# Performance work log

Hardware: AMD Instinct MI355X
Metric: run time of the kernel (lower is better)

Reference implementation:

```python
import jax, jax.numpy as jnp
import numpy as np

N = 100000      # nodes per node type (asset, zone)
E = 1000000     # edges per edge type
HID = 64        # hidden_dim
HEADS = 2
CH = HID // HEADS  # 32, GATConv out_channels per head
L = 2           # num_layers
A = 64          # action_count
NG = 6          # global features
FW = 2 * HID + NG  # 134 feature width for heads


def _gat(xs_in, xd_in, W, a_src, a_dst, bias, src, dst, n_dst):
    """PyG GATConv (v1, add_self_loops=False, concat=True) for one edge type.
    xs_in: [Ns, HID] source feats, xd_in: [Nd, HID] dest feats (same lin weight W).
    Returns [n_dst, HEADS*CH]."""
    xs = (xs_in @ W).reshape(-1, HEADS, CH)
    xd = (xd_in @ W).reshape(-1, HEADS, CH)
    al_s = jnp.einsum('nhc,hc->nh', xs, a_src)
    al_d = jnp.einsum('nhc,hc->nh', xd, a_dst)
    al = jax.nn.leaky_relu(al_s[src] + al_d[dst], 0.2)       # [E, H]
    mx = jax.ops.segment_max(al, dst, num_segments=n_dst)    # segment softmax (stable)
    mx = jnp.where(jnp.isfinite(mx), mx, 0.0)                # empty segments
    ex = jnp.exp(al - mx[dst])
    den = jax.ops.segment_sum(ex, dst, num_segments=n_dst)
    w = ex / (den[dst] + 1e-16)                              # PyG softmax eps
    msg = xs[src] * w[:, :, None]                            # [E, H, C]
    out = jax.ops.segment_sum(msg.reshape(msg.shape[0], HEADS * CH), dst, num_segments=n_dst)
    return out + bias


def setup_inputs() -> dict:
    key = jax.random.key(0)
    ks = jax.random.split(key, 24)
    s = 0.05
    inp = {
        'x_asset': jax.random.normal(ks[0], (N, 16), jnp.float32),
        'x_zone': jax.random.normal(ks[1], (N, 32), jnp.float32),
        'ei_zz': jax.random.randint(ks[2], (2, E), 0, N, dtype=jnp.int32),
        'ei_az': jax.random.randint(ks[3], (2, E), 0, N, dtype=jnp.int32),
        'ei_za': jax.random.randint(ks[4], (2, E), 0, N, dtype=jnp.int32),
        'gvec': jax.random.uniform(ks[5], (NG,), jnp.float32),
        'mask': jax.random.randint(ks[6], (A,), 0, 2) == 1,
        'proj_W_asset': jax.random.normal(ks[7], (16, HID), jnp.float32) * s,
        'proj_b_asset': jnp.zeros((HID,), jnp.float32),
        'proj_W_zone': jax.random.normal(ks[8], (32, HID), jnp.float32) * s,
        'proj_b_zone': jnp.zeros((HID,), jnp.float32),
        'gat_W': jax.random.normal(ks[9], (L, 3, HID, HID), jnp.float32) * s,
        'gat_asrc': jax.random.normal(ks[10], (L, 3, HEADS, CH), jnp.float32) * s,
        'gat_adst': jax.random.normal(ks[11], (L, 3, HEADS, CH), jnp.float32) * s,
        'gat_bias': jnp.zeros((L, 3, HID), jnp.float32),
        'actor_W1': jax.random.normal(ks[12], (FW, HID), jnp.float32) * s,
        'actor_b1': jnp.zeros((HID,), jnp.float32),
        'actor_W2': jax.random.normal(ks[13], (HID, A), jnp.float32) * s,
        'actor_b2': jnp.zeros((A,), jnp.float32),
        'critic_W1': jax.random.normal(ks[14], (FW, HID), jnp.float32) * s,
        'critic_b1': jnp.zeros((HID,), jnp.float32),
        'critic_W2': jax.random.normal(ks[15], (HID, 1), jnp.float32) * s,
        'critic_b2': jnp.zeros((1,), jnp.float32),
    }
    return inp


def reference(x_asset, x_zone, ei_zz, ei_az, ei_za, gvec, mask,
              proj_W_asset, proj_b_asset, proj_W_zone, proj_b_zone,
              gat_W, gat_asrc, gat_adst, gat_bias,
              actor_W1, actor_b1, actor_W2, actor_b2,
              critic_W1, critic_b1, critic_W2, critic_b2):
    # input projections per node type
    ha = x_asset @ proj_W_asset + proj_b_asset   # [N, HID]
    hz = x_zone @ proj_W_zone + proj_b_zone      # [N, HID]
    # HeteroConv stack: edge types 0=(zone,near,zone) 1=(asset,in,zone) 2=(zone,contains,asset), aggr='sum'
    for l in range(L):
        z_zz = _gat(hz, hz, gat_W[l, 0], gat_asrc[l, 0], gat_adst[l, 0], gat_bias[l, 0], ei_zz[0], ei_zz[1], N)
        z_az = _gat(ha, hz, gat_W[l, 1], gat_asrc[l, 1], gat_adst[l, 1], gat_bias[l, 1], ei_az[0], ei_az[1], N)
        a_za = _gat(hz, ha, gat_W[l, 2], gat_asrc[l, 2], gat_adst[l, 2], gat_bias[l, 2], ei_za[0], ei_za[1], N)
        hz = jax.nn.relu(z_zz + z_az)
        ha = jax.nn.relu(a_za)
    # mean pool per node type, sorted order: asset, zone
    pooled = jnp.concatenate([ha.mean(axis=0), hz.mean(axis=0)])
    feats = jnp.concatenate([pooled, gvec])      # [FW]
    logits = jax.nn.relu(feats @ actor_W1 + actor_b1) @ actor_W2 + actor_b2   # [A]
    value = jax.nn.relu(feats @ critic_W1 + critic_b1) @ critic_W2 + critic_b2  # [1]
    m = jnp.where(mask.any(), mask, jnp.ones_like(mask))
    masked = jnp.where(m, logits, -jnp.inf)
    return jnp.concatenate([masked, value])      # [A+1]: masked logits + value
```

## Files before the change

kernel.cpp:

```cpp
#include <hip/hip_runtime.h>
#include <math.h>

#define CE 8192
#define BSH 9
#define BMAXB 512
#define ASTR 104
#define DSTR 72

typedef __attribute__((ext_vector_type(8))) short bf16x8;
typedef __attribute__((ext_vector_type(4))) float f32x4;
typedef __attribute__((ext_vector_type(2))) float f32x2;

__device__ __forceinline__ unsigned short f2bf(float f) {
    unsigned u = __float_as_uint(f);
    u += 0x7fffu + ((u >> 16) & 1u);
    return (unsigned short)(u >> 16);
}
__device__ __forceinline__ float bf2f(unsigned short u) {
    return __uint_as_float(((unsigned)u) << 16);
}

__global__ __launch_bounds__(256) void gemm2_k(const float* __restrict__ Xa,
                                               const float* __restrict__ Xz,
                                               const float* __restrict__ Wa,
                                               const float* __restrict__ Wz,
                                               const float* __restrict__ ba,
                                               const float* __restrict__ bz,
                                               unsigned short* __restrict__ outa,
                                               unsigned short* __restrict__ outz,
                                               int n) {
    const int y = blockIdx.y;
    const float* X = y ? Xz : Xa;
    const float* W = y ? Wz : Wa;
    const float* bias = y ? bz : ba;
    unsigned short* outb = y ? outz : outa;
    const int kshift = y ? 5 : 4;
    const int K = 1 << kshift;

    __shared__ float sXt[64 * 68];
    __shared__ float sW[64 * 64];
    __shared__ float sB[64];
    const int tid = threadIdx.x;
    const int row0 = blockIdx.x * 64;

    for (int i = tid * 4; i < 64 * K; i += 1024) {
        int r = i >> kshift, k = i & (K - 1);
        int row = row0 + r;
        float4 v = make_float4(0.f, 0.f, 0.f, 0.f);
        if (row < n) v = *(const float4*)(X + (size_t)row * K + k);
        sXt[(k + 0) * 68 + r] = v.x;
        sXt[(k + 1) * 68 + r] = v.y;
        sXt[(k + 2) * 68 + r] = v.z;
        sXt[(k + 3) * 68 + r] = v.w;
    }
    for (int i = tid * 4; i < K * 64; i += 1024)
        *(float4*)(sW + i) = *(const float4*)(W + i);
    if (tid < 64) sB[tid] = bias[tid];
    __syncthreads();

    const int tc = tid & 15, tr = tid >> 4;
    float acc[4][4] = {};
#pragma unroll 8
    for (int k = 0; k < K; ++k) {
        float4 a = *(const float4*)(sXt + k * 68 + tr * 4);
        float4 b = *(const float4*)(sW + k * 64 + tc * 4);
        acc[0][0] += a.x * b.x; acc[0][1] += a.x * b.y; acc[0][2] += a.x * b.z; acc[0][3] += a.x * b.w;
        acc[1][0] += a.y * b.x; acc[1][1] += a.y * b.y; acc[1][2] += a.y * b.z; acc[1][3] += a.y * b.w;
        acc[2][0] += a.z * b.x; acc[2][1] += a.z * b.y; acc[2][2] += a.z * b.z; acc[2][3] += a.z * b.w;
        acc[3][0] += a.w * b.x; acc[3][1] += a.w * b.y; acc[3][2] += a.w * b.z; acc[3][3] += a.w * b.w;
    }
#pragma unroll
    for (int i = 0; i < 4; ++i) {
        int row = row0 + tr * 4 + i;
        if (row < n) {
            float4 o;
            o.x = acc[i][0] + sB[tc * 4 + 0];
            o.y = acc[i][1] + sB[tc * 4 + 1];
            o.z = acc[i][2] + sB[tc * 4 + 2];
            o.w = acc[i][3] + sB[tc * 4 + 3];
            ushort4 v4 = make_ushort4(f2bf(o.x), f2bf(o.y), f2bf(o.z), f2bf(o.w));
            *(ushort4*)(outb + (size_t)row * 64 + tc * 4) = v4;
        }
    }
}

__global__ void prep_k(const float* __restrict__ gW, const float* __restrict__ gad,
                       unsigned short* __restrict__ Wbt, float* __restrict__ Wd3All) {
    int b = blockIdx.x;
    int t = threadIdx.x;
    if (b < 6) {
        for (int i = t; i < 4096; i += 384) {
            int nn = i >> 6, k = i & 63;
            Wbt[(size_t)b * 4096 + i] = f2bf(gW[(size_t)b * 4096 + k * 64 + nn]);
        }
    } else {
        int l = b - 6;
        int et = t >> 7, r = t & 127;
        int k = r >> 1, h = r & 1;
        const float* W = gW + (size_t)l * 3 * 4096 + et * 4096;
        const float* adst = gad + (size_t)l * 3 * 64 + et * 64;
        float s = 0.f;
        for (int c = 0; c < 32; ++c) s += W[k * 64 + h * 32 + c] * adst[h * 32 + c];
        Wd3All[l * 384 + t] = s;
    }
}

__global__ __launch_bounds__(256) void gemm_mfma3_k(const unsigned short* __restrict__ hzb,
                                                    const unsigned short* __restrict__ hab,
                                                    const unsigned short* __restrict__ WbtL,
                                                    const float* __restrict__ gasL,
                                                    const float* __restrict__ Wd3,
                                                    unsigned char* __restrict__ ts0,
                                                    unsigned char* __restrict__ ts1,
                                                    unsigned char* __restrict__ ts2,
                                                    float2* __restrict__ als0,
                                                    float2* __restrict__ als1,
                                                    float2* __restrict__ als2,
                                                    float2* __restrict__ ald_zz,
                                                    float2* __restrict__ ald_az,
                                                    float2* __restrict__ ald_za, int n) {
    const int et = blockIdx.y;
    const unsigned short* Xb = (et == 1) ? hab : hzb;
    const unsigned short* Wt = WbtL + (size_t)et * 4096;
    const float* asrc = gasL + et * 64;
    unsigned char* ts8 = (et == 0) ? ts0 : (et == 1) ? ts1 : ts2;
    float2* alsOut = (et == 0) ? als0 : (et == 1) ? als1 : als2;

    __shared__ unsigned short sA[64 * ASTR];
    __shared__ unsigned short sB[64 * ASTR];
    __shared__ float sAs[64];
    __shared__ float sWd[384];
    const int tid = threadIdx.x;
    const int row0 = blockIdx.x * 64;

    for (int i = tid; i < 512; i += 256) {
        int r = i >> 3, seg = i & 7;
        int row = row0 + r;
        uint4 v = make_uint4(0, 0, 0, 0);
        if (row < n) v = *(const uint4*)(Xb + (size_t)row * 64 + seg * 8);
        *(uint4*)(sA + r * ASTR + seg * 8) = v;
    }
    for (int i = tid; i < 512; i += 256) {
        int nn = i >> 3, seg = i & 7;
        *(uint4*)(sB + nn * ASTR + seg * 8) = *(const uint4*)(Wt + nn * 64 + seg * 8);
    }
    if (tid < 64) sAs[tid] = asrc[tid];
    for (int i = tid; i < 384; i += 256) sWd[i] = Wd3[i];
    __syncthreads();

    const int lane = tid & 63;
    const int w = tid >> 6;
    const int m = lane & 15, q = lane >> 4;

    bf16x8 a0 = *(const bf16x8*)(sA + (w * 16 + m) * ASTR + q * 8);
    bf16x8 a1 = *(const bf16x8*)(sA + (w * 16 + m) * ASTR + 32 + q * 8);
    f32x4 acc[4];
#pragma unroll
    for (int c = 0; c < 4; ++c) {
        bf16x8 b0 = *(const bf16x8*)(sB + (c * 16 + m) * ASTR + q * 8);
        bf16x8 b1 = *(const bf16x8*)(sB + (c * 16 + m) * ASTR + 32 + q * 8);
        f32x4 z = {0.f, 0.f, 0.f, 0.f};
        z = __builtin_amdgcn_mfma_f32_16x16x32_bf16(a0, b0, z, 0, 0, 0);
        z = __builtin_amdgcn_mfma_f32_16x16x32_bf16(a1, b1, z, 0, 0, 0);
        acc[c] = z;
    }
    float s0[4], s1[4];
#pragma unroll
    for (int r = 0; r < 4; ++r) {
        s0[r] = acc[0][r] * sAs[m] + acc[1][r] * sAs[16 + m];
        s1[r] = acc[2][r] * sAs[32 + m] + acc[3][r] * sAs[48 + m];
    }
#pragma unroll
    for (int off = 1; off < 16; off <<= 1) {
#pragma unroll
        for (int r = 0; r < 4; ++r) { s0[r] += __shfl_xor(s0[r], off); s1[r] += __shfl_xor(s1[r], off); }
    }
    if (m < 4) {
        int row = row0 + w * 16 + q * 4 + m;
        if (row < n) alsOut[row] = make_float2(s0[m], s1[m]);
    }

    if (et != 2) {
        const int rid = tid >> 2, part = tid & 3;
        const int row = row0 + rid;
        const unsigned short* rp = sA + rid * ASTR + part * 16;
        bf16x8 x0 = *(const bf16x8*)rp;
        bf16x8 x1 = *(const bf16x8*)(rp + 8);
        float xv[16];
#pragma unroll
        for (int i = 0; i < 8; ++i) {
            xv[i]     = bf2f((unsigned short)x0[i]);
            xv[8 + i] = bf2f((unsigned short)x1[i]);
        }
        const float* wd = sWd + (et == 0 ? 0 : 256);
        float p0 = 0.f, p1 = 0.f, t0 = 0.f, t1 = 0.f;
#pragma unroll
        for (int i = 0; i < 16; ++i) {
            int k = part * 16 + i;
            p0 += xv[i] * wd[2 * k];
            p1 += xv[i] * wd[2 * k + 1];
        }
        if (et == 0) {
#pragma unroll
            for (int i = 0; i < 16; ++i) {
                int k = part * 16 + i;
                t0 += xv[i] * sWd[128 + 2 * k];
                t1 += xv[i] * sWd[128 + 2 * k + 1];
            }
        }
        p0 += __shfl_xor(p0, 1); p0 += __shfl_xor(p0, 2);
        p1 += __shfl_xor(p1, 1); p1 += __shfl_xor(p1, 2);
        t0 += __shfl_xor(t0, 1); t0 += __shfl_xor(t0, 2);
        t1 += __shfl_xor(t1, 1); t1 += __shfl_xor(t1, 2);
        if (part == 0 && row < n) {
            if (et == 0) {
                ald_zz[row] = make_float2(p0, p1);
                ald_az[row] = make_float2(t0, t1);
            } else {
                ald_za[row] = make_float2(p0, p1);
            }
        }
    }

    __syncthreads();
    unsigned char* sD = (unsigned char*)sA;
    const int s = m & 3;
    const int rowx = ((s & 1) << 1) | (s >> 1);
    const int colb = (m & ~3);
#pragma unroll
    for (int c = 0; c < 4; ++c) {
        int pk01 = __builtin_amdgcn_cvt_pk_fp8_f32(acc[c][0], acc[c][1], 0, false);
        int pk23 = __builtin_amdgcn_cvt_pk_fp8_f32(acc[c][2], acc[c][3], 0, false);
        unsigned D = ((unsigned)pk01 & 0xFFFFu) | ((unsigned)pk23 << 16);
        unsigned P = (unsigned)__shfl_xor((int)D, 1);
        unsigned A = (s & 1) ? __builtin_amdgcn_perm(D, P, 0x07030602u)
                             : __builtin_amdgcn_perm(D, P, 0x01050004u);
        unsigned Q = (unsigned)__shfl_xor((int)A, 2);
        unsigned B = (s & 2) ? __builtin_amdgcn_perm(A, Q, 0x07060302u)
                             : __builtin_amdgcn_perm(A, Q, 0x01000504u);
        int rb = w * 16 + q * 4;
        *(unsigned*)(sD + (rb + rowx) * DSTR + c * 16 + colb) = B;
    }
    __syncthreads();
    for (int i = tid; i < 512; i += 256) {
        int r = i >> 3, seg = i & 7;
        int row = row0 + r;
        if (row < n)
            *(uint2*)(ts8 + (size_t)row * 64 + seg * 8) = *(const uint2*)(sD + r * DSTR + seg * 8);
    }
}

__global__ __launch_bounds__(1024) void chunk_hist_k(const int* __restrict__ e0p,
                                                     const int* __restrict__ e1p,
                                                     const int* __restrict__ e2p,
                                                     int* __restrict__ cnt,
                                                     int E, int CB, int NBr) {
    int b = blockIdx.x;
    int et = b / CB, c = b - et * CB;
    const int* dst = (et == 0 ? e0p : et == 1 ? e1p : e2p) + E;
    __shared__ int lcnt[BMAXB];
    int t = threadIdx.x;
    for (int i = t; i < NBr; i += 1024) lcnt[i] = 0;
    __syncthreads();
    int base = c * CE;
    for (int i = t; i < CE; i += 1024) {
        int e = base + i;
        if (e < E) atomicAdd(&lcnt[dst[e] >> BSH], 1);
    }
    __syncthreads();
    int rowbase = et * NBr;
    for (int i = t; i < NBr; i += 1024) cnt[(size_t)(rowbase + i) * CB + c] = lcnt[i];
}
__global__ __launch_bounds__(256) void row_scan_k(int* __restrict__ cnt,
                                                  int* __restrict__ btot, int CB) {
    size_t row = (size_t)blockIdx.x * CB;
    __shared__ int buf[512];
    int t = threadIdx.x;
    int o0 = (t < CB) ? cnt[row + t] : 0;
    int o1 = (t + 256 < CB) ? cnt[row + t + 256] : 0;
    buf[t] = o0; buf[t + 256] = o1;
    __syncthreads();
    for (int off = 1; off < 512; off <<= 1) {
        int v0 = (t >= off) ? buf[t - off] : 0;
        int v1 = (t + 256 >= off) ? buf[t + 256 - off] : 0;
        __syncthreads();
        buf[t] += v0; buf[t + 256] += v1;
        __syncthreads();
    }
    if (t < CB) cnt[row + t] = buf[t] - o0;
    if (t + 256 < CB) cnt[row + t + 256] = buf[t + 256] - o1;
    if (t == 0) btot[blockIdx.x] = buf[511];
}
__global__ __launch_bounds__(1024) void btot_scan_k(const int* __restrict__ btot,
                                                    int* __restrict__ bbase,
                                                    int* __restrict__ bOff,
                                                    int NT, int E,
                                                    int* __restrict__ rowptrAll, int N) {
    __shared__ int buf[1024];
    int t = threadIdx.x;
    int v = (t < NT) ? btot[t] : 0;
    buf[t] = v;
    __syncthreads();
    for (int off = 1; off < 1024; off <<= 1) {
        int u = (t >= off) ? buf[t - off] : 0;
        __syncthreads();
        buf[t] += u;
        __syncthreads();
    }
    if (t < NT) { int e = buf[t] - v; bbase[t] = e; bOff[t] = e; }
    if (t == 0) {
        bOff[NT] = 3 * E;
        rowptrAll[N] = E;
        rowptrAll[(N + 1) + N] = 2 * E;
        rowptrAll[2 * (N + 1) + N] = 3 * E;
    }
}
__global__ __launch_bounds__(1024) void chunk_scatter_k(const int* __restrict__ e0p,
                                                        const int* __restrict__ e1p,
                                                        const int* __restrict__ e2p,
                                                        const int* __restrict__ cnt,
                                                        const int* __restrict__ bbase,
                                                        int* __restrict__ pairs,
                                                        int E, int CB, int NBr) {
    int b = blockIdx.x;
    int et = b / CB, c = b - et * CB;
    const int* eb = (et == 0 ? e0p : et == 1 ? e1p : e2p);
    __shared__ int lhist[BMAXB];
    __shared__ int lcur[BMAXB];
    __shared__ int wsum[16];
    __shared__ int lbuf[CE];
    __shared__ int tgt[CE];
    int t = threadIdx.x;
    int rb = et * NBr;
    for (int i = t; i < NBr; i += 1024) lhist[i] = 0;
    __syncthreads();
    int base = c * CE;
    int d[8], sv[8];
#pragma unroll
    for (int k = 0; k < 8; ++k) {
        int e = base + t + k * 1024;
        bool live = e < E;
        d[k] = live ? eb[E + e] : -1;
        sv[k] = live ? eb[e] : 0;
        if (live) atomicAdd(&lhist[d[k] >> BSH], 1);
    }
    __syncthreads();
    int v = (t < NBr) ? lhist[t] : 0;
    int x = v;
#pragma unroll
    for (int off = 1; off < 64; off <<= 1) {
        int u = __shfl_up(x, off);
        if ((t & 63) >= off) x += u;
    }
    if ((t & 63) == 63) wsum[t >> 6] = x;
    __syncthreads();
    int basep = 0;
#pragma unroll
    for (int qq = 0; qq < 16; ++qq) basep += (qq < (t >> 6)) ? wsum[qq] : 0;
    int myofs = basep + x - v;
    __syncthreads();
    if (t < NBr) {
        lcur[t] = myofs;
        lhist[t] = bbase[rb + t] + cnt[(size_t)(rb + t) * CB + c] - myofs;
    }
    __syncthreads();
#pragma unroll
    for (int k = 0; k < 8; ++k) {
        if (d[k] >= 0) {
            int bkt = d[k] >> BSH;
            int pos = atomicAdd(&lcur[bkt], 1);
            lbuf[pos] = ((d[k] & (BMAXB - 1)) << 20) | sv[k];
            tgt[pos] = lhist[bkt];
        }
    }
    __syncthreads();
    int tot = min(CE, E - base);
    for (int p = t; p < tot; p += 1024)
        pairs[tgt[p] + p] = lbuf[p];
}
__global__ __launch_bounds__(512) void bucket_local_k(const int* __restrict__ pairs,
                                                      const int* __restrict__ bOff,
                                                      int* __restrict__ rowptrAll,
                                                      int* __restrict__ ssrc, int N, int NBr) {
    int b = blockIdx.x;
    int et = b / NBr, lb = b - et * NBr;
    int beg = bOff[b], end = bOff[b + 1];
    int node0 = lb << BSH;
    int* rowptr = rowptrAll + (size_t)et * (N + 1);
    __shared__ int deg[512];
    __shared__ int cur[512];
    __shared__ int wsum[8];
    __shared__ int lbuf[8192];
    int t = threadIdx.x, lane = t & 63, wq = t >> 6;
    deg[t] = 0;
    __syncthreads();
    for (int j = beg + t; j < end; j += 512)
        atomicAdd(&deg[pairs[j] >> 20], 1);
    __syncthreads();
    int v = deg[t];
    int x = v;
#pragma unroll
    for (int off = 1; off < 64; off <<= 1) {
        int u = __shfl_up(x, off);
        if (lane >= off) x += u;
    }
    if (lane == 63) wsum[wq] = x;
    __syncthreads();
    int basep = 0;
#pragma unroll
    for (int q = 0; q < 8; ++q) basep += (q < wq) ? wsum[q] : 0;
    int localofs = basep + x - v;
    int nedge = end - beg;
    bool useLds = nedge <= 8192;
    cur[t] = useLds ? localofs : beg + localofs;
    int n0 = node0 + t;
    if (n0 < N) rowptr[n0] = beg + localofs;
    __syncthreads();
    if (useLds) {
        for (int j = beg + t; j < end; j += 512) {
            int p = pairs[j];
            int pos = atomicAdd(&cur[p >> 20], 1);
            lbuf[pos] = p & 0xFFFFF;
        }
        __syncthreads();
        for (int p = t; p < nedge; p += 512)
            ssrc[beg + p] = lbuf[p];
    } else {
        for (int j = beg + t; j < end; j += 512) {
            int p = pairs[j];
            int pos = atomicAdd(&cur[p >> 20], 1);
            ssrc[pos] = p & 0xFFFFF;
        }
    }
}

__global__ __launch_bounds__(256) void gat_out2_k(const int* __restrict__ rowptr0,
                                                  const int* __restrict__ rowptr1,
                                                  const int* __restrict__ rowptr2,
                                                  const int* __restrict__ ssrc,
                                                  const float2* __restrict__ als0,
                                                  const float2* __restrict__ ald0,
                                                  const unsigned char* __restrict__ ts0,
                                                  const float2* __restrict__ als1,
                                                  const float2* __restrict__ ald1,
                                                  const unsigned char* __restrict__ ts1,
                                                  const float2* __restrict__ als2,
                                                  const float2* __restrict__ ald2,
                                                  const unsigned char* __restrict__ ts2,
                                                  const float* __restrict__ gbL,
                                                  unsigned short* __restrict__ outHz,
                                                  unsigned short* __restrict__ outHa,
                                                  int n) {
    const int y = blockIdx.y;
    const int nseg = y ? 1 : 2;
    int lane = threadIdx.x & 63;
    int gl = lane & 15;
    int wid = blockIdx.x * 16 + (threadIdx.x >> 4);
    if (wid >= n) return;
    const int r = gl >> 3;
    const int c0 = (gl & 7) * 8;
    const int gbase = lane & 48;

    float acc8[8] = {};
    for (int seg = 0; seg < nseg; ++seg) {
        const int* rowptr;
        const float2 *als, *ald;
        const unsigned char* ts8;
        if (y) { rowptr = rowptr2; als = als2; ald = ald2; ts8 = ts2; }
        else if (seg == 0) { rowptr = rowptr0; als = als0; ald = ald0; ts8 = ts0; }
        else { rowptr = rowptr1; als = als1; ald = ald1; ts8 = ts1; }
        int beg = rowptr[wid], end = rowptr[wid + 1];
        if (beg == end) continue;
        float2 bd = ald[wid];
        float d0 = 0.f, d1 = 0.f;
        float a8[8] = {};
        for (int cbeg = beg; cbeg < end; cbeg += 16) {
            int j = cbeg + gl;
            int s = 0; float e0 = 0.f, e1 = 0.f;
            if (j < end) {
                s = ssrc[j];
                float2 a = als[s];
                float l0 = a.x + bd.x; l0 = l0 > 0.f ? l0 : 0.2f * l0;
                float l1 = a.y + bd.y; l1 = l1 > 0.f ? l1 : 0.2f * l1;
                e0 = __expf(l0); e1 = __expf(l1);
            }
            d0 += e0; d1 += e1;
            int cnt = min(16, end - cbeg);
            uint2 rr[8]; float wv[8];
#pragma unroll
            for (int k = 0; k < 8; ++k) {
                int jj = 2 * k;
                if (jj < cnt) {
                    int srcLane = gbase + jj + r;
                    int sj = __shfl(s, srcLane);
                    float w0 = __shfl(e0, srcLane), w1 = __shfl(e1, srcLane);
                    float w = (c0 < 32) ? w0 : w1;
                    bool live = (jj + r) < cnt;
                    wv[k] = live ? w : 0.f;
                    if (live) rr[k] = *(const uint2*)(ts8 + (size_t)sj * 64 + c0);
                    else rr[k] = make_uint2(0, 0);
                } else { wv[k] = 0.f; rr[k] = make_uint2(0, 0); }
            }
#pragma unroll
            for (int k = 0; k < 8; ++k) {
                float w = wv[k];
                if (w != 0.f) {
                    f32x2 p0 = __builtin_amdgcn_cvt_pk_f32_fp8(rr[k].x, false);
                    f32x2 p1 = __builtin_amdgcn_cvt_pk_f32_fp8(rr[k].x, true);
                    f32x2 p2 = __builtin_amdgcn_cvt_pk_f32_fp8(rr[k].y, false);
                    f32x2 p3 = __builtin_amdgcn_cvt_pk_f32_fp8(rr[k].y, true);
                    a8[0] += p0.x * w; a8[1] += p0.y * w;
                    a8[2] += p1.x * w; a8[3] += p1.y * w;
                    a8[4] += p2.x * w; a8[5] += p2.y * w;
                    a8[6] += p3.x * w; a8[7] += p3.y * w;
                }
            }
        }
#pragma unroll
        for (int off = 1; off < 16; off <<= 1) { d0 += __shfl_xor(d0, off); d1 += __shfl_xor(d1, off); }
#pragma unroll
        for (int i = 0; i < 8; ++i) a8[i] += __shfl_xor(a8[i], 8);
        float inv = (c0 < 32) ? 1.f / (d0 + 1e-16f) : 1.f / (d1 + 1e-16f);
#pragma unroll
        for (int i = 0; i < 8; ++i) acc8[i] += a8[i] * inv;
    }

    if (r == 0) {
        const float* biasA = y ? gbL + 128 : gbL;
        const float* biasB = y ? nullptr : gbL + 64;
        float4 bA1 = *(const float4*)(biasA + c0);
        float4 bA2 = *(const float4*)(biasA + c0 + 4);
        float b8[8] = { bA1.x, bA1.y, bA1.z, bA1.w, bA2.x, bA2.y, bA2.z, bA2.w };
        if (biasB) {
            float4 bB1 = *(const float4*)(biasB + c0);
            float4 bB2 = *(const float4*)(biasB + c0 + 4);
            b8[0] += bB1.x; b8[1] += bB1.y; b8[2] += bB1.z; b8[3] += bB1.w;
            b8[4] += bB2.x; b8[5] += bB2.y; b8[6] += bB2.z; b8[7] += bB2.w;
        }
        float v8[8];
#pragma unroll
        for (int i = 0; i < 8; ++i) v8[i] = fmaxf(acc8[i] + b8[i], 0.f);
        unsigned short* outBf = y ? outHa : outHz;
        unsigned short* bp = outBf + (size_t)wid * 64 + c0;
        ushort4 u1 = make_ushort4(f2bf(v8[0]), f2bf(v8[1]), f2bf(v8[2]), f2bf(v8[3]));
        ushort4 u2 = make_ushort4(f2bf(v8[4]), f2bf(v8[5]), f2bf(v8[6]), f2bf(v8[7]));
        *(ushort4*)bp = u1;
        *(ushort4*)(bp + 4) = u2;
    }
}

__global__ __launch_bounds__(256) void pool_k(const unsigned short* __restrict__ hab,
                                              const unsigned short* __restrict__ hzb,
                                              float* __restrict__ sums, int n) {
    __shared__ float red[2][16][64];
    int tid = threadIdx.x;
    int c4 = (tid & 15) * 4;
    int rq = tid >> 4;
    float la[4] = {}, lz[4] = {};
    for (int row = blockIdx.x * 16 + rq; row < n; row += gridDim.x * 16) {
        ushort4 va = *(const ushort4*)(hab + (size_t)row * 64 + c4);
        ushort4 vz = *(const ushort4*)(hzb + (size_t)row * 64 + c4);
        la[0] += bf2f(va.x); la[1] += bf2f(va.y); la[2] += bf2f(va.z); la[3] += bf2f(va.w);
        lz[0] += bf2f(vz.x); lz[1] += bf2f(vz.y); lz[2] += bf2f(vz.z); lz[3] += bf2f(vz.w);
    }
#pragma unroll
    for (int i = 0; i < 4; ++i) { red[0][rq][c4 + i] = la[i]; red[1][rq][c4 + i] = lz[i]; }
    __syncthreads();
    if (tid < 64) {
        float ta = 0.f, tz = 0.f;
#pragma unroll
        for (int rr = 0; rr < 16; ++rr) { ta += red[0][rr][tid]; tz += red[1][rr][tid]; }
        atomicAdd(sums + tid, ta);
        atomicAdd(sums + 64 + tid, tz);
    }
}

__global__ __launch_bounds__(64) void head_k(const float* __restrict__ sums,
                                             const float* __restrict__ gvec,
                                             const unsigned char* __restrict__ mask,
                                             const float* __restrict__ aW1, const float* __restrict__ ab1,
                                             const float* __restrict__ aW2, const float* __restrict__ ab2,
                                             const float* __restrict__ cW1, const float* __restrict__ cb1,
                                             const float* __restrict__ cW2, const float* __restrict__ cb2,
                                             float* __restrict__ out, float invn) {
    __shared__ float f[134];
    __shared__ float h1a[64];
    int t = threadIdx.x;
    f[t] = sums[t] * invn;
    f[64 + t] = sums[64 + t] * invn;
    if (t < 6) f[128 + t] = gvec[t];
    __syncthreads();
    float a = ab1[t], c = cb1[t];
    for (int i = 0; i < 134; ++i) {
        float fv = f[i];
        a += fv * aW1[i * 64 + t];
        c += fv * cW1[i * 64 + t];
    }
    h1a[t] = fmaxf(a, 0.f);
    float vp = fmaxf(c, 0.f) * cW2[t];
    __syncthreads();
    float lg = ab2[t];
    for (int j = 0; j < 64; ++j) lg += h1a[j] * aW2[j * 64 + t];
    for (int off = 32; off; off >>= 1) vp += __shfl_down(vp, off);
    unsigned char mb = mask[t];
    unsigned long long bal = __ballot(mb != 0);
    float ov = (bal == 0ull || mb) ? lg : -3.0e38f;
    out[t] = ov;
    if (t == 0) out[64] = vp + cb2[0];
}

extern "C" void kernel_launch(void* const* d_in, const int* in_sizes, int n_in,
                              void* d_out, int out_size, void* d_ws, size_t ws_size,
                              hipStream_t stream) {
    const float* x_asset = (const float*)d_in[0];
    const float* x_zone  = (const float*)d_in[1];
    const int* ei[3] = { (const int*)d_in[2], (const int*)d_in[3], (const int*)d_in[4] };
    const float* gvec = (const float*)d_in[5];
    const unsigned char* mask = (const unsigned char*)d_in[6];
    const float* pWa = (const float*)d_in[7];
    const float* pba = (const float*)d_in[8];
    const float* pWz = (const float*)d_in[9];
    const float* pbz = (const float*)d_in[10];
    const float* gW  = (const float*)d_in[11];
    const float* gas = (const float*)d_in[12];
    const float* gad = (const float*)d_in[13];
    const float* gb  = (const float*)d_in[14];
    const float* aW1 = (const float*)d_in[15];
    const float* ab1 = (const float*)d_in[16];
    const float* aW2 = (const float*)d_in[17];
    const float* ab2 = (const float*)d_in[18];
    const float* cW1 = (const float*)d_in[19];
    const float* cb1 = (const float*)d_in[20];
    const float* cW2 = (const float*)d_in[21];
    const float* cb2 = (const float*)d_in[22];

    const int N = in_sizes[0] / 16;
    const int E = in_sizes[2] / 2;
    const int NBr = (N + 511) >> BSH;
    const int CB  = (E + CE - 1) / CE;
    const int NT  = 3 * NBr;

    float* ws = (float*)d_ws;
    size_t off = 0;
    unsigned short* hab = (unsigned short*)(ws + off); off += (size_t)N * 32;
    unsigned short* hzb = (unsigned short*)(ws + off); off += (size_t)N * 32;
    unsigned char* ts3[3];
    for (int et = 0; et < 3; ++et) { ts3[et] = (unsigned char*)(ws + off); off += (size_t)N * 16; }
    float2* als3[3];
    for (int et = 0; et < 3; ++et) { als3[et] = (float2*)(ws + off); off += (size_t)2 * N; }
    float2* ald3[3];
    for (int et = 0; et < 3; ++et) { ald3[et] = (float2*)(ws + off); off += (size_t)2 * N; }
    unsigned short* Wbt = (unsigned short*)(ws + off); off += 12288 + 64;
    float* Wd3All = ws + off; off += 768;
    float* sums = ws + off; off += 128;
    int* rowptrAll = (int*)(ws + off); off += (size_t)3 * (N + 1);
    int* ssrcAll   = (int*)(ws + off); off += (size_t)3 * E;
    int* pairs     = (int*)(ws + off); off += (size_t)3 * E;
    int* cnt   = (int*)(ws + off); off += (size_t)NT * CB;
    int* btot  = (int*)(ws + off); off += 1024;
    int* bbase = (int*)(ws + off); off += 1024;
    int* bOff  = (int*)(ws + off); off += (size_t)(NT + 1);

    const int gGemm = (N + 63) / 64;
    const int gGat  = (N + 15) / 16;

    chunk_hist_k<<<3 * CB, 1024, 0, stream>>>(ei[0], ei[1], ei[2], cnt, E, CB, NBr);
    row_scan_k<<<NT, 256, 0, stream>>>(cnt, btot, CB);
    btot_scan_k<<<1, 1024, 0, stream>>>(btot, bbase, bOff, NT, E, rowptrAll, N);
    chunk_scatter_k<<<3 * CB, 1024, 0, stream>>>(ei[0], ei[1], ei[2], cnt, bbase, pairs, E, CB, NBr);
    bucket_local_k<<<NT, 512, 0, stream>>>(pairs, bOff, rowptrAll, ssrcAll, N, NBr);

    prep_k<<<8, 384, 0, stream>>>(gW, gad, Wbt, Wd3All);
    gemm2_k<<<dim3(gGemm, 2), 256, 0, stream>>>(x_asset, x_zone, pWa, pWz, pba, pbz,
                                                hab, hzb, N);

    for (int l = 0; l < 2; ++l) {
        gemm_mfma3_k<<<dim3(gGemm, 3), 256, 0, stream>>>(hzb, hab,
                                                         Wbt + (size_t)l * 3 * 4096,
                                                         gas + (size_t)l * 3 * 64,
                                                         Wd3All + (size_t)l * 384,
                                                         ts3[0], ts3[1], ts3[2],
                                                         als3[0], als3[1], als3[2],
                                                         ald3[0], ald3[1], ald3[2], N);
        gat_out2_k<<<dim3(gGat, 2), 256, 0, stream>>>(rowptrAll, rowptrAll + (N + 1),
                                                      rowptrAll + 2 * (N + 1), ssrcAll,
                                                      als3[0], ald3[0], ts3[0],
                                                      als3[1], ald3[1], ts3[1],
                                                      als3[2], ald3[2], ts3[2],
                                                      gb + (size_t)l * 3 * 64,
                                                      hzb, hab, N);
    }

    hipMemsetAsync(sums, 0, 128 * sizeof(float), stream);
    pool_k<<<256, 256, 0, stream>>>(hab, hzb, sums, N);
    head_k<<<1, 64, 0, stream>>>(sums, gvec, mask,
                                 aW1, ab1, aW2, ab2, cW1, cb1, cW2, cb2,
                                 (float*)d_out, 1.0f / (float)N);
}
```

Baseline: 378.7 us.

## Share zone-feature tile across two edge-type GEMMs and fuse pooling into last GAT

The per-layer GEMM now launches two y-slices instead of three. The zone slice loads the hz tile once and computes both the zz and za projections, which removes a redundant read of hz and one block-row of launches. The final GAT aggregation layer skips writing bf16 node features and instead writes per-block column partial sums, so pool_k reduces the small partial arrays rather than rereading all node features. The cost is more shared memory and registers per GEMM block, an uneven amount of work between the two y-slices, and added LDS reduction plus syncthreads in the last GAT kernel.

```diff
diff --git a/kernel.cpp b/kernel.cpp
--- a/kernel.cpp
+++ b/kernel.cpp
@@ -105,6 +105,27 @@
     }
 }
 
+__device__ __forceinline__ void stage_fp8(const f32x4* acc, unsigned char* sD,
+                                          int w, int q, int m) {
+    const int s = m & 3;
+    const int rowx = ((s & 1) << 1) | (s >> 1);
+    const int colb = (m & ~3);
+#pragma unroll
+    for (int c = 0; c < 4; ++c) {
+        int pk01 = __builtin_amdgcn_cvt_pk_fp8_f32(acc[c][0], acc[c][1], 0, false);
+        int pk23 = __builtin_amdgcn_cvt_pk_fp8_f32(acc[c][2], acc[c][3], 0, false);
+        unsigned D = ((unsigned)pk01 & 0xFFFFu) | ((unsigned)pk23 << 16);
+        unsigned P = (unsigned)__shfl_xor((int)D, 1);
+        unsigned A = (s & 1) ? __builtin_amdgcn_perm(D, P, 0x07030602u)
+                             : __builtin_amdgcn_perm(D, P, 0x01050004u);
+        unsigned Q = (unsigned)__shfl_xor((int)A, 2);
+        unsigned B = (s & 2) ? __builtin_amdgcn_perm(A, Q, 0x07060302u)
+                             : __builtin_amdgcn_perm(A, Q, 0x01000504u);
+        int rb = w * 16 + q * 4;
+        *(unsigned*)(sD + (rb + rowx) * DSTR + c * 16 + colb) = B;
+    }
+}
+
 __global__ __launch_bounds__(256) void gemm_mfma3_k(const unsigned short* __restrict__ hzb,
                                                     const unsigned short* __restrict__ hab,
                                                     const unsigned short* __restrict__ WbtL,
@@ -119,16 +140,15 @@
                                                     float2* __restrict__ ald_zz,
                                                     float2* __restrict__ ald_az,
                                                     float2* __restrict__ ald_za, int n) {
-    const int et = blockIdx.y;
-    const unsigned short* Xb = (et == 1) ? hab : hzb;
-    const unsigned short* Wt = WbtL + (size_t)et * 4096;
-    const float* asrc = gasL + et * 64;
-    unsigned char* ts8 = (et == 0) ? ts0 : (et == 1) ? ts1 : ts2;
-    float2* alsOut = (et == 0) ? als0 : (et == 1) ? als1 : als2;
+    const int y = blockIdx.y;
+    const unsigned short* Xb = y ? hab : hzb;
+    const unsigned short* WtA = WbtL + (size_t)(y ? 1 : 0) * 4096;
+    const unsigned short* WtC = WbtL + (size_t)2 * 4096;
 
     __shared__ unsigned short sA[64 * ASTR];
-    __shared__ unsigned short sB[64 * ASTR];
-    __shared__ float sAs[64];
+    __shared__ unsigned short sB0[64 * ASTR];
+    __shared__ unsigned short sB2[64 * ASTR];
+    __shared__ float sAs[128];
     __shared__ float sWd[384];
     const int tid = threadIdx.x;
     const int row0 = blockIdx.x * 64;
@@ -142,9 +162,15 @@
     }
     for (int i = tid; i < 512; i += 256) {
         int nn = i >> 3, seg = i & 7;
-        *(uint4*)(sB + nn * ASTR + seg * 8) = *(const uint4*)(Wt + nn * 64 + seg * 8);
-    }
-    if (tid < 64) sAs[tid] = asrc[tid];
+        *(uint4*)(sB0 + nn * ASTR + seg * 8) = *(const uint4*)(WtA + nn * 64 + seg * 8);
+    }
+    if (y == 0)
+        for (int i = tid; i < 512; i += 256) {
+            int nn = i >> 3, seg = i & 7;
+            *(uint4*)(sB2 + nn * ASTR + seg * 8) = *(const uint4*)(WtC + nn * 64 + seg * 8);
+        }
+    if (tid < 64) sAs[tid] = gasL[(y ? 1 : 0) * 64 + tid];
+    if (y == 0 && tid >= 64 && tid < 128) sAs[tid] = gasL[2 * 64 + (tid - 64)];
     for (int i = tid; i < 384; i += 256) sWd[i] = Wd3[i];
     __syncthreads();
 
@@ -154,33 +180,64 @@
 
     bf16x8 a0 = *(const bf16x8*)(sA + (w * 16 + m) * ASTR + q * 8);
     bf16x8 a1 = *(const bf16x8*)(sA + (w * 16 + m) * ASTR + 32 + q * 8);
-    f32x4 acc[4];
+    f32x4 accA[4], accC[4];
 #pragma unroll
     for (int c = 0; c < 4; ++c) {
-        bf16x8 b0 = *(const bf16x8*)(sB + (c * 16 + m) * ASTR + q * 8);
-        bf16x8 b1 = *(const bf16x8*)(sB + (c * 16 + m) * ASTR + 32 + q * 8);
+        bf16x8 b0 = *(const bf16x8*)(sB0 + (c * 16 + m) * ASTR + q * 8);
+        bf16x8 b1 = *(const bf16x8*)(sB0 + (c * 16 + m) * ASTR + 32 + q * 8);
         f32x4 z = {0.f, 0.f, 0.f, 0.f};
         z = __builtin_amdgcn_mfma_f32_16x16x32_bf16(a0, b0, z, 0, 0, 0);
         z = __builtin_amdgcn_mfma_f32_16x16x32_bf16(a1, b1, z, 0, 0, 0);
-        acc[c] = z;
-    }
-    float s0[4], s1[4];
-#pragma unroll
-    for (int r = 0; r < 4; ++r) {
-        s0[r] = acc[0][r] * sAs[m] + acc[1][r] * sAs[16 + m];
-        s1[r] = acc[2][r] * sAs[32 + m] + acc[3][r] * sAs[48 + m];
-    }
-#pragma unroll
-    for (int off = 1; off < 16; off <<= 1) {
-#pragma unroll
-        for (int r = 0; r < 4; ++r) { s0[r] += __shfl_xor(s0[r], off); s1[r] += __shfl_xor(s1[r], off); }
-    }
-    if (m < 4) {
-        int row = row0 + w * 16 + q * 4 + m;
-        if (row < n) alsOut[row] = make_float2(s0[m], s1[m]);
-    }
-
-    if (et != 2) {
+        accA[c] = z;
+    }
+    if (y == 0) {
+#pragma unroll
+        for (int c = 0; c < 4; ++c) {
+            bf16x8 b0 = *(const bf16x8*)(sB2 + (c * 16 + m) * ASTR + q * 8);
+            bf16x8 b1 = *(const bf16x8*)(sB2 + (c * 16 + m) * ASTR + 32 + q * 8);
+            f32x4 z = {0.f, 0.f, 0.f, 0.f};
+            z = __builtin_amdgcn_mfma_f32_16x16x32_bf16(a0, b0, z, 0, 0, 0);
+            z = __builtin_amdgcn_mfma_f32_16x16x32_bf16(a1, b1, z, 0, 0, 0);
+            accC[c] = z;
+        }
+    }
+
+    {
+        float s0[4], s1[4];
+#pragma unroll
+        for (int r = 0; r < 4; ++r) {
+            s0[r] = accA[0][r] * sAs[m] + accA[1][r] * sAs[16 + m];
+            s1[r] = accA[2][r] * sAs[32 + m] + accA[3][r] * sAs[48 + m];
+        }
+#pragma unroll
+        for (int off = 1; off < 16; off <<= 1) {
+#pragma unroll
+            for (int r = 0; r < 4; ++r) { s0[r] += __shfl_xor(s0[r], off); s1[r] += __shfl_xor(s1[r], off); }
+        }
+        if (m < 4) {
+            int row = row0 + w * 16 + q * 4 + m;
+            if (row < n) (y ? als1 : als0)[row] = make_float2(s0[m], s1[m]);
+        }
+    }
+    if (y == 0) {
+        float s0[4], s1[4];
+#pragma unroll
+        for (int r = 0; r < 4; ++r) {
+            s0[r] = accC[0][r] * sAs[64 + m] + accC[1][r] * sAs[80 + m];
+            s1[r] = accC[2][r] * sAs[96 + m] + accC[3][r] * sAs[112 + m];
+        }
+#pragma unroll
+        for (int off = 1; off < 16; off <<= 1) {
+#pragma unroll
+            for (int r = 0; r < 4; ++r) { s0[r] += __shfl_xor(s0[r], off); s1[r] += __shfl_xor(s1[r], off); }
+        }
+        if (m < 4) {
+            int row = row0 + w * 16 + q * 4 + m;
+            if (row < n) als2[row] = make_float2(s0[m], s1[m]);
+        }
+    }
+
+    {
         const int rid = tid >> 2, part = tid & 3;
         const int row = row0 + rid;
         const unsigned short* rp = sA + rid * ASTR + part * 16;
@@ -192,7 +249,7 @@
             xv[i]     = bf2f((unsigned short)x0[i]);
             xv[8 + i] = bf2f((unsigned short)x1[i]);
         }
-        const float* wd = sWd + (et == 0 ? 0 : 256);
+        const float* wd = (y == 0) ? sWd : sWd + 256;
         float p0 = 0.f, p1 = 0.f, t0 = 0.f, t1 = 0.f;
 #pragma unroll
         for (int i = 0; i < 16; ++i) {
@@ -200,7 +257,7 @@
             p0 += xv[i] * wd[2 * k];
             p1 += xv[i] * wd[2 * k + 1];
         }
-        if (et == 0) {
+        if (y == 0) {
 #pragma unroll
             for (int i = 0; i < 16; ++i) {
                 int k = part * 16 + i;
@@ -213,7 +270,7 @@
         t0 += __shfl_xor(t0, 1); t0 += __shfl_xor(t0, 2);
         t1 += __shfl_xor(t1, 1); t1 += __shfl_xor(t1, 2);
         if (part == 0 && row < n) {
-            if (et == 0) {
+            if (y == 0) {
                 ald_zz[row] = make_float2(p0, p1);
                 ald_az[row] = make_float2(t0, t1);
             } else {
@@ -224,29 +281,25 @@
 
     __syncthreads();
     unsigned char* sD = (unsigned char*)sA;
-    const int s = m & 3;
-    const int rowx = ((s & 1) << 1) | (s >> 1);
-    const int colb = (m & ~3);
-#pragma unroll
-    for (int c = 0; c < 4; ++c) {
-        int pk01 = __builtin_amdgcn_cvt_pk_fp8_f32(acc[c][0], acc[c][1], 0, false);
-        int pk23 = __builtin_amdgcn_cvt_pk_fp8_f32(acc[c][2], acc[c][3], 0, false);
-        unsigned D = ((unsigned)pk01 & 0xFFFFu) | ((unsigned)pk23 << 16);
-        unsigned P = (unsigned)__shfl_xor((int)D, 1);
-        unsigned A = (s & 1) ? __builtin_amdgcn_perm(D, P, 0x07030602u)
-                             : __builtin_amdgcn_perm(D, P, 0x01050004u);
-        unsigned Q = (unsigned)__shfl_xor((int)A, 2);
-        unsigned B = (s & 2) ? __builtin_amdgcn_perm(A, Q, 0x07060302u)
-                             : __builtin_amdgcn_perm(A, Q, 0x01000504u);
-        int rb = w * 16 + q * 4;
-        *(unsigned*)(sD + (rb + rowx) * DSTR + c * 16 + colb) = B;
-    }
-    __syncthreads();
+    stage_fp8(accA, sD, w, q, m);
+    __syncthreads();
+    unsigned char* tsA = y ? ts1 : ts0;
     for (int i = tid; i < 512; i += 256) {
         int r = i >> 3, seg = i & 7;
         int row = row0 + r;
         if (row < n)
-            *(uint2*)(ts8 + (size_t)row * 64 + seg * 8) = *(const uint2*)(sD + r * DSTR + seg * 8);
+            *(uint2*)(tsA + (size_t)row * 64 + seg * 8) = *(const uint2*)(sD + r * DSTR + seg * 8);
+    }
+    if (y == 0) {
+        __syncthreads();
+        stage_fp8(accC, sD, w, q, m);
+        __syncthreads();
+        for (int i = tid; i < 512; i += 256) {
+            int r = i >> 3, seg = i & 7;
+            int row = row0 + r;
+            if (row < n)
+                *(uint2*)(ts2 + (size_t)row * 64 + seg * 8) = *(const uint2*)(sD + r * DSTR + seg * 8);
+        }
     }
 }
 
@@ -450,18 +503,25 @@
                                                   const float* __restrict__ gbL,
                                                   unsigned short* __restrict__ outHz,
                                                   unsigned short* __restrict__ outHa,
+                                                  float* __restrict__ pool0,
+                                                  float* __restrict__ pool1,
                                                   int n) {
     const int y = blockIdx.y;
     const int nseg = y ? 1 : 2;
     int lane = threadIdx.x & 63;
     int gl = lane & 15;
-    int wid = blockIdx.x * 16 + (threadIdx.x >> 4);
-    if (wid >= n) return;
+    int grp = threadIdx.x >> 4;
+    int wid = blockIdx.x * 16 + grp;
+    const bool pooling = (pool0 != nullptr);
+    if (!pooling && wid >= n) return;
+    const bool act = wid < n;
     const int r = gl >> 3;
     const int c0 = (gl & 7) * 8;
     const int gbase = lane & 48;
+    __shared__ float sPool[16][64];
 
     float acc8[8] = {};
+    if (act)
     for (int seg = 0; seg < nseg; ++seg) {
         const int* rowptr;
         const float2 *als, *ald;
@@ -526,50 +586,62 @@
     }
 
     if (r == 0) {
-        const float* biasA = y ? gbL + 128 : gbL;
-        const float* biasB = y ? nullptr : gbL + 64;
-        float4 bA1 = *(const float4*)(biasA + c0);
-        float4 bA2 = *(const float4*)(biasA + c0 + 4);
-        float b8[8] = { bA1.x, bA1.y, bA1.z, bA1.w, bA2.x, bA2.y, bA2.z, bA2.w };
-        if (biasB) {
-            float4 bB1 = *(const float4*)(biasB + c0);
-            float4 bB2 = *(const float4*)(biasB + c0 + 4);
-            b8[0] += bB1.x; b8[1] += bB1.y; b8[2] += bB1.z; b8[3] += bB1.w;
-            b8[4] += bB2.x; b8[5] += bB2.y; b8[6] += bB2.z; b8[7] += bB2.w;
-        }
-        float v8[8];
-#pragma unroll
-        for (int i = 0; i < 8; ++i) v8[i] = fmaxf(acc8[i] + b8[i], 0.f);
-        unsigned short* outBf = y ? outHa : outHz;
-        unsigned short* bp = outBf + (size_t)wid * 64 + c0;
-        ushort4 u1 = make_ushort4(f2bf(v8[0]), f2bf(v8[1]), f2bf(v8[2]), f2bf(v8[3]));
-        ushort4 u2 = make_ushort4(f2bf(v8[4]), f2bf(v8[5]), f2bf(v8[6]), f2bf(v8[7]));
-        *(ushort4*)bp = u1;
-        *(ushort4*)(bp + 4) = u2;
-    }
-}
-
-__global__ __launch_bounds__(256) void pool_k(const unsigned short* __restrict__ hab,
-                                              const unsigned short* __restrict__ hzb,
-                                              float* __restrict__ sums, int n) {
-    __shared__ float red[2][16][64];
+        float v8[8] = {0.f, 0.f, 0.f, 0.f, 0.f, 0.f, 0.f, 0.f};
+        if (act) {
+            const float* biasA = y ? gbL + 128 : gbL;
+            const float* biasB = y ? nullptr : gbL + 64;
+            float4 bA1 = *(const float4*)(biasA + c0);
+            float4 bA2 = *(const float4*)(biasA + c0 + 4);
+            float b8[8] = { bA1.x, bA1.y, bA1.z, bA1.w, bA2.x, bA2.y, bA2.z, bA2.w };
+            if (biasB) {
+                float4 bB1 = *(const float4*)(biasB + c0);
+                float4 bB2 = *(const float4*)(biasB + c0 + 4);
+                b8[0] += bB1.x; b8[1] += bB1.y; b8[2] += bB1.z; b8[3] += bB1.w;
+                b8[4] += bB2.x; b8[5] += bB2.y; b8[6] += bB2.z; b8[7] += bB2.w;
+            }
+#pragma unroll
+            for (int i = 0; i < 8; ++i) v8[i] = fmaxf(acc8[i] + b8[i], 0.f);
+        }
+        if (pooling) {
+#pragma unroll
+            for (int i = 0; i < 8; ++i) sPool[grp][c0 + i] = v8[i];
+        } else {
+            unsigned short* outBf = y ? outHa : outHz;
+            unsigned short* bp = outBf + (size_t)wid * 64 + c0;
+            ushort4 u1 = make_ushort4(f2bf(v8[0]), f2bf(v8[1]), f2bf(v8[2]), f2bf(v8[3]));
+            ushort4 u2 = make_ushort4(f2bf(v8[4]), f2bf(v8[5]), f2bf(v8[6]), f2bf(v8[7]));
+            *(ushort4*)bp = u1;
+            *(ushort4*)(bp + 4) = u2;
+        }
+    }
+    if (pooling) {
+        __syncthreads();
+        int t = threadIdx.x;
+        if (t < 64) {
+            float s = 0.f;
+#pragma unroll
+            for (int g = 0; g < 16; ++g) s += sPool[g][t];
+            (y ? pool1 : pool0)[(size_t)blockIdx.x * 64 + t] = s;
+        }
+    }
+}
+
+__global__ __launch_bounds__(256) void pool_k(const float* __restrict__ part0,
+                                              const float* __restrict__ part1,
+                                              float* __restrict__ sums, int nblk) {
+    __shared__ float red[2][4][64];
     int tid = threadIdx.x;
-    int c4 = (tid & 15) * 4;
-    int rq = tid >> 4;
-    float la[4] = {}, lz[4] = {};
-    for (int row = blockIdx.x * 16 + rq; row < n; row += gridDim.x * 16) {
-        ushort4 va = *(const ushort4*)(hab + (size_t)row * 64 + c4);
-        ushort4 vz = *(const ushort4*)(hzb + (size_t)row * 64 + c4);
-        la[0] += bf2f(va.x); la[1] += bf2f(va.y); la[2] += bf2f(va.z); la[3] += bf2f(va.w);
-        lz[0] += bf2f(vz.x); lz[1] += bf2f(vz.y); lz[2] += bf2f(vz.z); lz[3] += bf2f(vz.w);
-    }
-#pragma unroll
-    for (int i = 0; i < 4; ++i) { red[0][rq][c4 + i] = la[i]; red[1][rq][c4 + i] = lz[i]; }
+    int col = tid & 63, rq = tid >> 6;
+    float sa = 0.f, sz = 0.f;
+    for (int row = blockIdx.x * 4 + rq; row < nblk; row += gridDim.x * 4) {
+        sa += part1[(size_t)row * 64 + col];
+        sz += part0[(size_t)row * 64 + col];
+    }
+    red[0][rq][col] = sa; red[1][rq][col] = sz;
     __syncthreads();
     if (tid < 64) {
-        float ta = 0.f, tz = 0.f;
-#pragma unroll
-        for (int rr = 0; rr < 16; ++rr) { ta += red[0][rr][tid]; tz += red[1][rr][tid]; }
+        float ta = red[0][0][tid] + red[0][1][tid] + red[0][2][tid] + red[0][3][tid];
+        float tz = red[1][0][tid] + red[1][1][tid] + red[1][2][tid] + red[1][3][tid];
         atomicAdd(sums + tid, ta);
         atomicAdd(sums + 64 + tid, tz);
     }
@@ -640,6 +712,9 @@
     const int CB  = (E + CE - 1) / CE;
     const int NT  = 3 * NBr;
 
+    const int gGemm = (N + 63) / 64;
+    const int gGat  = (N + 15) / 16;
+
     float* ws = (float*)d_ws;
     size_t off = 0;
     unsigned short* hab = (unsigned short*)(ws + off); off += (size_t)N * 32;
@@ -653,6 +728,8 @@
     unsigned short* Wbt = (unsigned short*)(ws + off); off += 12288 + 64;
     float* Wd3All = ws + off; off += 768;
     float* sums = ws + off; off += 128;
+    float* part0 = ws + off; off += (size_t)gGat * 64;
+    float* part1 = ws + off; off += (size_t)gGat * 64;
     int* rowptrAll = (int*)(ws + off); off += (size_t)3 * (N + 1);
     int* ssrcAll   = (int*)(ws + off); off += (size_t)3 * E;
     int* pairs     = (int*)(ws + off); off += (size_t)3 * E;
@@ -661,9 +738,6 @@
     int* bbase = (int*)(ws + off); off += 1024;
     int* bOff  = (int*)(ws + off); off += (size_t)(NT + 1);
 
-    const int gGemm = (N + 63) / 64;
-    const int gGat  = (N + 15) / 16;
-
     chunk_hist_k<<<3 * CB, 1024, 0, stream>>>(ei[0], ei[1], ei[2], cnt, E, CB, NBr);
     row_scan_k<<<NT, 256, 0, stream>>>(cnt, btot, CB);
     btot_scan_k<<<1, 1024, 0, stream>>>(btot, bbase, bOff, NT, E, rowptrAll, N);
@@ -675,24 +749,27 @@
                                                 hab, hzb, N);
 
     for (int l = 0; l < 2; ++l) {
-        gemm_mfma3_k<<<dim3(gGemm, 3), 256, 0, stream>>>(hzb, hab,
+        gemm_mfma3_k<<<dim3(gGemm, 2), 256, 0, stream>>>(hzb, hab,
                                                          Wbt + (size_t)l * 3 * 4096,
                                                          gas + (size_t)l * 3 * 64,
                                                          Wd3All + (size_t)l * 384,
                                                          ts3[0], ts3[1], ts3[2],
                                                          als3[0], als3[1], als3[2],
                                                          ald3[0], ald3[1], ald3[2], N);
+        const bool fin = (l == 1);
         gat_out2_k<<<dim3(gGat, 2), 256, 0, stream>>>(rowptrAll, rowptrAll + (N + 1),
                                                       rowptrAll + 2 * (N + 1), ssrcAll,
                                                       als3[0], ald3[0], ts3[0],
                                                       als3[1], ald3[1], ts3[1],
                                                       als3[2], ald3[2], ts3[2],
                                                       gb + (size_t)l * 3 * 64,
-                                                      hzb, hab, N);
+                                                      hzb, hab,
+                                                      fin ? part0 : nullptr,
+                                                      fin ? part1 : nullptr, N);
     }
 
     hipMemsetAsync(sums, 0, 128 * sizeof(float), stream);
-    pool_k<<<256, 256, 0, stream>>>(hab, hzb, sums, N);
+    pool_k<<<64, 256, 0, stream>>>(part0, part1, sums, gGat);
     head_k<<<1, 64, 0, stream>>>(sums, gvec, mask,
                                  aW1, ab1, aW2, ab2, cW1, cb1, cW2, cb2,
                                  (float*)d_out, 1.0f / (float)N);
```

Result: slower. 391.3 us (+3.3%).
